# Kernel tuning notes

Hardware: AMD Instinct MI355X
Metric: run time of the kernel (lower is better)

## Reference

```python
import jax, jax.numpy as jnp
import numpy as np

B, S, D, H = 4, 2048, 768, 12
DK = D // H


def setup_inputs() -> dict:
    key = jax.random.key(0)
    ks = jax.random.split(key, 13)
    s = 1.0 / np.sqrt(D)
    inp = {
        "q": jax.random.normal(ks[0], (B, S, D), jnp.float32),
        "k": jax.random.normal(ks[1], (B, S, D), jnp.float32),
        "v": jax.random.normal(ks[2], (B, S, D), jnp.float32),
        "mask": jax.random.randint(ks[3], (B, S), 0, 2, jnp.int32),
        "Wq": jax.random.normal(ks[4], (D, D), jnp.float32) * s,
        "bq": jnp.zeros((D,), jnp.float32),
        "Wk": jax.random.normal(ks[5], (D, D), jnp.float32) * s,
        "bk": jnp.zeros((D,), jnp.float32),
        "Wv": jax.random.normal(ks[6], (D, D), jnp.float32) * s,
        "bv": jnp.zeros((D,), jnp.float32),
        "Wo": jax.random.normal(ks[7], (D, D), jnp.float32) * s,
        "bo": jnp.zeros((D,), jnp.float32),
    }
    return inp


def reference(q, k, v, mask, Wq, bq, Wk, bk, Wv, bv, Wo, bo):
    b, s, d = q.shape
    # projections (torch Linear: x @ W.T + b), split into heads: [b, h, s, dk]
    Q = (q @ Wq.T + bq).reshape(b, s, H, DK).transpose(0, 2, 1, 3)
    K = (k @ Wk.T + bk).reshape(b, s, H, DK).transpose(0, 2, 1, 3)
    V = (v @ Wv.T + bv).reshape(b, s, H, DK).transpose(0, 2, 1, 3)
    scores = jnp.einsum("bhqd,bhkd->bhqk", Q, K) / jnp.sqrt(jnp.float32(DK))
    # mask [b,s] -> [b,1,s,1]: masks whole query rows (faithful to source)
    scores = jnp.where(mask[:, None, :, None] == 0, jnp.float32(-1e9), scores)
    attn = jax.nn.softmax(scores, axis=-1)  # dropout is identity at inference
    out = jnp.einsum("bhqk,bhkd->bhqd", attn, V)
    concat = out.transpose(0, 2, 1, 3).reshape(b, s, d)
    return concat @ Wo.T + bo
```

## Files before the change

kernel.cpp:

```cpp
#include <hip/hip_runtime.h>

typedef _Float16 f16;
typedef f16 f16x2 __attribute__((ext_vector_type(2)));
typedef f16 f16x4 __attribute__((ext_vector_type(4)));
typedef f16 f16x8 __attribute__((ext_vector_type(8)));
typedef float f32x4 __attribute__((ext_vector_type(4)));
typedef float f32x16 __attribute__((ext_vector_type(16)));

#define B_ 4
#define S_ 2048
#define D_ 768
#define H_ 12
#define DK_ 64

__device__ __forceinline__ void dma16(const f16* g, f16* l) {
    __builtin_amdgcn_global_load_lds(
        (__attribute__((address_space(1))) void*)(uintptr_t)g,
        (__attribute__((address_space(3))) void*)l, 16, 0, 0);
}

__device__ __forceinline__ float exp2_raw(float x) {
#if __has_builtin(__builtin_amdgcn_exp2f)
    return __builtin_amdgcn_exp2f(x);
#else
    float r; asm("v_exp_f32 %0, %1" : "=v"(r) : "v"(x)); return r;
#endif
}

struct Cvt7 { const float* s[7]; f16* d[7]; };

__global__ __launch_bounds__(256) void cvt7_kernel(Cvt7 a)
{
    const int chunk = blockIdx.x * 256 + threadIdx.x;
    int z; int local;
    if (chunk < 2359296) { z = chunk / 786432; local = chunk - z * 786432; }
    else { int c2 = chunk - 2359296; int zi = c2 / 73728; z = 3 + zi; local = c2 - zi * 73728; }
    const size_t i = (size_t)local * 8;
    const float* __restrict__ s = a.s[z];
    float4 x = *(const float4*)(s + i);
    float4 y = *(const float4*)(s + i + 4);
    f16x8 h = {(f16)x.x, (f16)x.y, (f16)x.z, (f16)x.w,
               (f16)y.x, (f16)y.y, (f16)y.z, (f16)y.w};
    *(f16x8*)(a.d[z] + i) = h;
}

struct GemmArgs { const f16* A; const f16* W; const float* bias; float scale; void* C; int mode; };
struct GemmArgs3 { GemmArgs g[3]; };

template <int MODE>
__global__ __launch_bounds__(256, 2) void gemm_t(GemmArgs3 args)
{
    const int z = blockIdx.z;
    const f16* __restrict__ A = args.g[z].A;
    const f16* __restrict__ W = args.g[z].W;
    const float* __restrict__ bias = args.g[z].bias;
    const float scale = args.g[z].scale;

    __shared__ __align__(16) f16 AB[2][2][8192];

    const int tid = threadIdx.x, lane = tid & 63, w = tid >> 6;
    const int l15 = lane & 15, lg = lane >> 4;
    const int wm = (w >> 1) * 64, wn = (w & 1) * 64;
    const int m0 = blockIdx.y * 128, n0 = blockIdx.x * 128;

    const int lrow8 = lane >> 3;
    const int lchk8 = (lane & 7) ^ lrow8;
    const f16* gA = A + (size_t)(m0 + w * 32 + lrow8) * D_ + lchk8 * 8;
    const f16* gB = W + (size_t)(n0 + w * 32 + lrow8) * D_ + lchk8 * 8;

#define GSTAGE(j)                                                             \
    {                                                                         \
        f16* Ad = &AB[(j) & 1][0][0];                                         \
        f16* Bd = &AB[(j) & 1][1][0];                                         \
        const int kts = (j) * 64;                                             \
        _Pragma("unroll")                                                     \
        for (int c = 0; c < 4; ++c) {                                         \
            dma16(gA + (size_t)(c * 8) * D_ + kts, &Ad[(w * 4 + c) * 512]);   \
            dma16(gB + (size_t)(c * 8) * D_ + kts, &Bd[(w * 4 + c) * 512]);   \
        }                                                                     \
    }

    GSTAGE(0);
    GSTAGE(1);

    f32x4 acc[4][4] = {};

#pragma unroll 2
    for (int t = 0; t < 12; ++t) {
        const f16* Asc = &AB[t & 1][0][0];
        const f16* Bsc = &AB[t & 1][1][0];

        if (t == 11) asm volatile("s_waitcnt vmcnt(0)" ::: "memory");
        else         asm volatile("s_waitcnt vmcnt(8)" ::: "memory");
        __builtin_amdgcn_s_barrier();

#pragma unroll
        for (int kk = 0; kk < 2; ++kk) {
            const int chk = ((kk * 4 + lg) ^ (l15 & 7)) * 8;
            f16x8 af[4], bf[4];
#pragma unroll
            for (int i = 0; i < 4; ++i)
                af[i] = *(const f16x8*)&Asc[(wm + i * 16 + l15) * 64 + chk];
#pragma unroll
            for (int j = 0; j < 4; ++j)
                bf[j] = *(const f16x8*)&Bsc[(wn + j * 16 + l15) * 64 + chk];
#pragma unroll
            for (int i = 0; i < 4; ++i)
#pragma unroll
                for (int j = 0; j < 4; ++j)
                    acc[i][j] = __builtin_amdgcn_mfma_f32_16x16x32_f16(
                        bf[j], af[i], acc[i][j], 0, 0, 0);
        }

        asm volatile("s_waitcnt lgkmcnt(0)" ::: "memory");
        __builtin_amdgcn_s_barrier();
        if (t + 2 < 12) GSTAGE(t + 2);
    }
#undef GSTAGE

    if constexpr (MODE == 0) {
        const int omode = args.g[z].mode;
        if (omode == 1) {
#pragma unroll
            for (int j = 0; j < 4; ++j) {
                int col = n0 + wn + j * 16 + lg * 4;
                float4 bb = *(const float4*)&bias[col];
#pragma unroll
                for (int i = 0; i < 4; ++i) {
                    int row = m0 + wm + i * 16 + l15;
                    int bI = row >> 11, sl = row & (S_ - 1);
                    f16* base = (f16*)args.g[z].C + (size_t)bI * D_ * S_ + sl;
                    base[(size_t)(col + 0) * S_] = (f16)(acc[i][j][0] + bb.x);
                    base[(size_t)(col + 1) * S_] = (f16)(acc[i][j][1] + bb.y);
                    base[(size_t)(col + 2) * S_] = (f16)(acc[i][j][2] + bb.z);
                    base[(size_t)(col + 3) * S_] = (f16)(acc[i][j][3] + bb.w);
                }
            }
        } else {
#pragma unroll
            for (int j = 0; j < 4; ++j) {
                int col = n0 + wn + j * 16 + lg * 4;
                float4 bb = *(const float4*)&bias[col];
#pragma unroll
                for (int i = 0; i < 4; ++i) {
                    int row = m0 + wm + i * 16 + l15;
                    f16x4 o = {(f16)((acc[i][j][0] + bb.x) * scale),
                               (f16)((acc[i][j][1] + bb.y) * scale),
                               (f16)((acc[i][j][2] + bb.z) * scale),
                               (f16)((acc[i][j][3] + bb.w) * scale)};
                    *(f16x4*)&((f16*)args.g[z].C)[(size_t)row * D_ + col] = o;
                }
            }
        }
    } else {
#pragma unroll
        for (int j = 0; j < 4; ++j) {
            int col = n0 + wn + j * 16 + lg * 4;
            float4 bb = *(const float4*)&bias[col];
#pragma unroll
            for (int i = 0; i < 4; ++i) {
                int row = m0 + wm + i * 16 + l15;
                float4 o = {acc[i][j][0] + bb.x, acc[i][j][1] + bb.y,
                            acc[i][j][2] + bb.z, acc[i][j][3] + bb.w};
                *(float4*)&((float*)args.g[z].C)[(size_t)row * D_ + col] = o;
            }
        }
    }
}

__global__ __launch_bounds__(256, 3) void attn_k(
    const f16* __restrict__ Qh, const f16* __restrict__ Kh,
    const f16* __restrict__ VhT, const int* __restrict__ mask,
    f16* __restrict__ O)
{
    __shared__ __align__(16) f16 lds[2][8192];
    const int tid = threadIdx.x, lane = tid & 63, w = tid >> 6;
    const int l31 = lane & 31, lhi = lane >> 5;

    const int bid = blockIdx.x;
    const int g8 = bid & 7, j5 = bid >> 3;
    const int head_lin = g8 * 6 + (j5 >> 4);
    const int qt = j5 & 15;
    const int b = head_lin / H_, h = head_lin % H_;
    const int q0 = qt * 128;
    const int rowbase = b * S_;
    const int col0 = h * DK_;

    const int lrow8 = lane >> 3;
    const int lchk8 = (lane & 7) ^ lrow8;

    {
        const f16* Qbase = Qh + (size_t)(rowbase + q0 + w * 32 + lrow8) * D_ + col0 + lchk8 * 8;
#pragma unroll
        for (int c = 0; c < 4; ++c)
            dma16(Qbase + (size_t)(c * 8) * D_, &lds[0][(w * 4 + c) * 512]);
    }
    __syncthreads();
    f16x8 qf[4];
    {
        const int qrow = w * 32 + l31;
        const f16 mf = (f16)((mask[rowbase + q0 + qrow] != 0) ? 1.0f : 0.0f);
#pragma unroll
        for (int dc = 0; dc < 4; ++dc) {
            f16x8 t = *(const f16x8*)&lds[0][qrow * 64 +
                                            (((dc * 2 + lhi) ^ (qrow & 7)) * 8)];
            qf[dc] = t * mf;
        }
    }
    __syncthreads();

    const f16* Kbase = Kh + (size_t)rowbase * D_ + col0;
    const f16* Vbase = VhT + ((size_t)b * D_ + col0) * S_;

#define STAGE(j)                                                              \
    {                                                                         \
        f16* Ksd = &lds[(j) & 1][0];                                          \
        f16* Vtd = &lds[(j) & 1][4096];                                       \
        const int k0s = (j) * 64;                                             \
        _Pragma("unroll")                                                     \
        for (int c = 0; c < 2; ++c) {                                         \
            int o = w * 2 + c;                                                \
            dma16(Kbase + (size_t)(k0s + o * 8 + lrow8) * D_ + lchk8 * 8,     \
                  &Ksd[o * 512]);                                             \
            dma16(Vbase + (size_t)(o * 8 + lrow8) * S_ + k0s + lchk8 * 8,     \
                  &Vtd[o * 512]);                                             \
        }                                                                     \
    }

    STAGE(0);
    STAGE(1);

    float rsum = 0.f;
    f32x16 acc[2] = {};

#pragma unroll 2
    for (int t = 0; t < 32; ++t) {
        const f16* Ksc = &lds[t & 1][0];
        const f16* Vtc = &lds[t & 1][4096];

        if (t == 31) asm volatile("s_waitcnt vmcnt(0)" ::: "memory");
        else         asm volatile("s_waitcnt vmcnt(4)" ::: "memory");
        __builtin_amdgcn_s_barrier();

#pragma unroll
        for (int kc = 0; kc < 2; ++kc) {
            f32x16 s = {};
            __builtin_amdgcn_s_setprio(1);
#pragma unroll
            for (int dc = 0; dc < 4; ++dc) {
                f16x8 kf = *(const f16x8*)&Ksc[(kc * 32 + l31) * 64 +
                                               (((dc * 2 + lhi) ^ (lane & 7)) * 8)];
                s = __builtin_amdgcn_mfma_f32_32x32x16_f16(kf, qf[dc], s, 0, 0, 0);
            }
            __builtin_amdgcn_s_setprio(0);
            f16x4 pb[4];
#pragma unroll
            for (int g = 0; g < 4; ++g) {
                float e0 = exp2_raw(s[4 * g + 0]);
                float e1 = exp2_raw(s[4 * g + 1]);
                float e2 = exp2_raw(s[4 * g + 2]);
                float e3 = exp2_raw(s[4 * g + 3]);
                rsum += (e0 + e1) + (e2 + e3);
                unsigned lo = __builtin_bit_cast(unsigned, __builtin_amdgcn_cvt_pkrtz(e0, e1));
                unsigned hi = __builtin_bit_cast(unsigned, __builtin_amdgcn_cvt_pkrtz(e2, e3));
                uint2 u; u.x = lo; u.y = hi;
                pb[g] = __builtin_bit_cast(f16x4, u);
            }
            __builtin_amdgcn_s_setprio(1);
#pragma unroll
            for (int g = 0; g < 4; ++g) {
                int kb = kc * 4 + g;
#pragma unroll
                for (int dc2 = 0; dc2 < 2; ++dc2) {
                    f16x4 vf = *(const f16x4*)&Vtc[(dc2 * 32 + l31) * 64 +
                                                   ((kb ^ (lane & 7)) * 8) + lhi * 4];
                    acc[dc2] = __builtin_amdgcn_mfma_f32_32x32x8f16(
                        vf, pb[g], acc[dc2], 0, 0, 0);
                }
            }
            __builtin_amdgcn_s_setprio(0);
        }

        asm volatile("s_waitcnt lgkmcnt(0)" ::: "memory");
        __builtin_amdgcn_s_barrier();
        if (t + 2 < 32) STAGE(t + 2);
    }

    rsum += __shfl_xor(rsum, 32, 64);
    const float inv = 1.0f / rsum;
    const size_t qrow = (size_t)(rowbase + q0 + w * 32 + l31);
#pragma unroll
    for (int dc2 = 0; dc2 < 2; ++dc2)
#pragma unroll
        for (int grp = 0; grp < 4; ++grp) {
            f16x4 ho = {(f16)(acc[dc2][4 * grp + 0] * inv),
                        (f16)(acc[dc2][4 * grp + 1] * inv),
                        (f16)(acc[dc2][4 * grp + 2] * inv),
                        (f16)(acc[dc2][4 * grp + 3] * inv)};
            *(f16x4*)&O[qrow * D_ + col0 + dc2 * 32 + grp * 8 + lhi * 4] = ho;
        }
#undef STAGE
}

extern "C" void kernel_launch(void* const* d_in, const int* in_sizes, int n_in,
                              void* d_out, int out_size, void* d_ws, size_t ws_size,
                              hipStream_t stream)
{
    const float* q    = (const float*)d_in[0];
    const float* k    = (const float*)d_in[1];
    const float* v    = (const float*)d_in[2];
    const int*   mask = (const int*)d_in[3];
    const float* Wq   = (const float*)d_in[4];
    const float* bq   = (const float*)d_in[5];
    const float* Wk   = (const float*)d_in[6];
    const float* bk   = (const float*)d_in[7];
    const float* Wv   = (const float*)d_in[8];
    const float* bv   = (const float*)d_in[9];
    const float* Wo   = (const float*)d_in[10];
    const float* bo   = (const float*)d_in[11];

    const size_t nQKV = (size_t)B_ * S_ * D_;
    const size_t nW   = (size_t)D_ * D_;

    f16* qh  = (f16*)d_ws;
    f16* kh  = qh + nQKV;
    f16* vh  = kh + nQKV;
    f16* Wqh = vh + nQKV;
    f16* Wkh = Wqh + nW;
    f16* Wvh = Wkh + nW;
    f16* Woh = Wvh + nW;
    f16* Qp  = Woh + nW;
    f16* Kp  = Qp + nQKV;
    f16* VpT = Kp + nQKV;
    f16* Cp  = VpT + nQKV;

    Cvt7 cv = {{q, k, v, Wq, Wk, Wv, Wo},
               {qh, kh, vh, Wqh, Wkh, Wvh, Woh}};
    cvt7_kernel<<<dim3(10368), 256, 0, stream>>>(cv);

    GemmArgs3 g1 = {{{qh, Wqh, bq, 1.44269504f / 8.0f, (void*)Qp, 0},
                     {kh, Wkh, bk, 1.0f, (void*)Kp, 0},
                     {vh, Wvh, bv, 1.0f, (void*)VpT, 1}}};
    gemm_t<0><<<dim3(6, 64, 3), 256, 0, stream>>>(g1);

    attn_k<<<dim3(768), 256, 0, stream>>>(Qp, Kp, VpT, mask, Cp);

    GemmArgs3 g2 = {{{Cp, Woh, bo, 1.0f, d_out, 2},
                     {Cp, Woh, bo, 1.0f, d_out, 2},
                     {Cp, Woh, bo, 1.0f, d_out, 2}}};
    gemm_t<2><<<dim3(6, 64, 1), 256, 0, stream>>>(g2);
}
```

Baseline: 274.2 us.

## Pre-swizzle K and V^T global layouts to reduce LDS bank conflicts in attention

```diff
diff --git a/kernel.cpp b/kernel.cpp
--- a/kernel.cpp
+++ b/kernel.cpp
@@ -125,15 +125,32 @@
             for (int j = 0; j < 4; ++j) {
                 int col = n0 + wn + j * 16 + lg * 4;
                 float4 bb = *(const float4*)&bias[col];
+                int swp = ((col >> 3) & 1) << 2;
 #pragma unroll
                 for (int i = 0; i < 4; ++i) {
                     int row = m0 + wm + i * 16 + l15;
-                    int bI = row >> 11, sl = row & (S_ - 1);
+                    int bI = row >> 11, sl = (row & (S_ - 1)) ^ swp;
                     f16* base = (f16*)args.g[z].C + (size_t)bI * D_ * S_ + sl;
                     base[(size_t)(col + 0) * S_] = (f16)(acc[i][j][0] + bb.x);
                     base[(size_t)(col + 1) * S_] = (f16)(acc[i][j][1] + bb.y);
                     base[(size_t)(col + 2) * S_] = (f16)(acc[i][j][2] + bb.z);
                     base[(size_t)(col + 3) * S_] = (f16)(acc[i][j][3] + bb.w);
+                }
+            }
+        } else if (omode == 2) {
+#pragma unroll
+            for (int j = 0; j < 4; ++j) {
+                int col = n0 + wn + j * 16 + lg * 4;
+                float4 bb = *(const float4*)&bias[col];
+#pragma unroll
+                for (int i = 0; i < 4; ++i) {
+                    int row = m0 + wm + i * 16 + l15;
+                    int csw = col ^ (((row >> 3) & 1) << 2);
+                    f16x4 o = {(f16)(acc[i][j][0] + bb.x),
+                               (f16)(acc[i][j][1] + bb.y),
+                               (f16)(acc[i][j][2] + bb.z),
+                               (f16)(acc[i][j][3] + bb.w)};
+                    *(f16x4*)&((f16*)args.g[z].C)[(size_t)row * D_ + csw] = o;
                 }
             }
         } else {
@@ -188,6 +205,8 @@
 
     const int lrow8 = lane >> 3;
     const int lchk8 = (lane & 7) ^ lrow8;
+    const int sigl = (lane & 7) ^ (((lane >> 4) & 1) << 2);
+    const int taul = (lane >> 3) & 1;
 
     {
         const f16* Qbase = Qh + (size_t)(rowbase + q0 + w * 32 + lrow8) * D_ + col0 + lchk8 * 8;
@@ -220,9 +239,10 @@
         _Pragma("unroll")                                                     \
         for (int c = 0; c < 2; ++c) {                                         \
             int o = w * 2 + c;                                                \
-            dma16(Kbase + (size_t)(k0s + o * 8 + lrow8) * D_ + lchk8 * 8,     \
+            int gc = lchk8 ^ (((o >> 1) & 1) << 2);                           \
+            dma16(Kbase + (size_t)(k0s + o * 8 + lrow8) * D_ + gc * 8,        \
                   &Ksd[o * 512]);                                             \
-            dma16(Vbase + (size_t)(o * 8 + lrow8) * S_ + k0s + lchk8 * 8,     \
+            dma16(Vbase + (size_t)(o * 8 + lrow8) * S_ + k0s + gc * 8,        \
                   &Vtd[o * 512]);                                             \
         }                                                                     \
     }
@@ -244,12 +264,15 @@
 
 #pragma unroll
         for (int kc = 0; kc < 2; ++kc) {
+            const int rowK = (kc * 32 + l31) * 64;
             f32x16 s = {};
             __builtin_amdgcn_s_setprio(1);
 #pragma unroll
             for (int dc = 0; dc < 4; ++dc) {
-                f16x8 kf = *(const f16x8*)&Ksc[(kc * 32 + l31) * 64 +
-                                               (((dc * 2 + lhi) ^ (lane & 7)) * 8)];
+                const int cb = (((dc * 2 + lhi) ^ sigl) << 3);
+                f16x4 klo = *(const f16x4*)&Ksc[rowK + cb + taul * 4];
+                f16x4 khi = *(const f16x4*)&Ksc[rowK + cb + (taul ^ 1) * 4];
+                f16x8 kf = __builtin_shufflevector(klo, khi, 0, 1, 2, 3, 4, 5, 6, 7);
                 s = __builtin_amdgcn_mfma_f32_32x32x16_f16(kf, qf[dc], s, 0, 0, 0);
             }
             __builtin_amdgcn_s_setprio(0);
@@ -270,10 +293,10 @@
 #pragma unroll
             for (int g = 0; g < 4; ++g) {
                 int kb = kc * 4 + g;
+                const int vslot = ((((kb ^ sigl) << 1) | (lhi ^ taul)) << 2);
 #pragma unroll
                 for (int dc2 = 0; dc2 < 2; ++dc2) {
-                    f16x4 vf = *(const f16x4*)&Vtc[(dc2 * 32 + l31) * 64 +
-                                                   ((kb ^ (lane & 7)) * 8) + lhi * 4];
+                    f16x4 vf = *(const f16x4*)&Vtc[(dc2 * 32 + l31) * 64 + vslot];
                     acc[dc2] = __builtin_amdgcn_mfma_f32_32x32x8f16(
                         vf, pb[g], acc[dc2], 0, 0, 0);
                 }
@@ -339,7 +362,7 @@
     cvt7_kernel<<<dim3(10368), 256, 0, stream>>>(cv);
 
     GemmArgs3 g1 = {{{qh, Wqh, bq, 1.44269504f / 8.0f, (void*)Qp, 0},
-                     {kh, Wkh, bk, 1.0f, (void*)Kp, 0},
+                     {kh, Wkh, bk, 1.0f, (void*)Kp, 2},
                      {vh, Wvh, bv, 1.0f, (void*)VpT, 1}}};
     gemm_t<0><<<dim3(6, 64, 3), 256, 0, stream>>>(g1);
 
```

New measurement: 293.4 us. 7.0% more time.
